# Kernel optimization log

Measured on AMD Instinct MI355X. Metric: run time of the kernel, lower is better.

The kernel has to match this reference:

```python
import jax, jax.numpy as jnp
import numpy as np

E = 7       # number of experts (len(expert_details))
K = 2       # top-k routing
CAP = 3072  # per-expert capacity ~ ceil(T*K/E * 1.25)
D = 1024    # d_model
H = 4096    # d_ff = 4*d_model
T = 8192    # tokens (B=2, S=4096)


def setup_inputs() -> dict:
    key = jax.random.key(0)
    k1, k2, k3, k4 = jax.random.split(key, 4)
    x = jax.random.normal(k1, (T, D), jnp.float32)
    Wg = jax.random.normal(k2, (D, E), jnp.float32) * 0.02
    W1 = jax.random.normal(k3, (E, D, H), jnp.float32) * 0.02
    W2 = jax.random.normal(k4, (E, H, D), jnp.float32) * 0.02
    return {"x": x, "Wg": Wg, "W1": W1, "W2": W2}


def reference(x, Wg, W1, W2):
    Tn, Dn = x.shape
    # --- router ---
    gates = jax.nn.softmax(x @ Wg, axis=-1)          # [T, E]
    topw, topi = jax.lax.top_k(gates, K)             # [T, K]
    topw = topw / jnp.sum(topw, axis=-1, keepdims=True)
    flat_e = topi.reshape(-1)                        # [T*K] expert ids (int)
    flat_w = topw.reshape(-1)                        # [T*K] combine weights
    # --- position within each expert (priority = token order) ---
    onehot = jax.nn.one_hot(flat_e, E, dtype=jnp.int32)           # [T*K, E]
    pos = jnp.sum(jnp.cumsum(onehot, axis=0) * onehot, axis=-1) - 1  # [T*K]
    keep = pos < CAP
    slot = jnp.where(keep, pos, CAP)  # overflow tokens go to pad slot CAP
    # --- dispatch: scatter tokens into [E, CAP, D] buffer ---
    x_rep = jnp.repeat(x, K, axis=0)                               # [T*K, D]
    buf = jnp.zeros((E, CAP + 1, Dn), x.dtype).at[flat_e, slot].set(x_rep)[:, :CAP]
    # --- grouped expert FFN (grouped GEMMs) ---
    h = jax.nn.gelu(jnp.einsum('ecd,edh->ech', buf, W1))
    y = jnp.einsum('ech,ehd->ecd', h, W2)                          # [E, CAP, D]
    # --- combine: gather back and weight ---
    y_pad = jnp.concatenate([y, jnp.zeros((E, 1, Dn), y.dtype)], axis=1)
    out_slots = y_pad[flat_e, slot] * (flat_w * keep.astype(flat_w.dtype))[:, None]
    return out_slots.reshape(Tn, K, Dn).sum(axis=1)                # [T, D]
```

## Files before the change

kernel.cpp:

```cpp
#include <hip/hip_runtime.h>
#include <stdint.h>


#define NEXP 7
#define KTOP 2
#define CAP 3072
#define DM 1024
#define HF 4096
#define TT 8192

typedef __bf16 bf16x8 __attribute__((ext_vector_type(8)));
typedef float f32x4 __attribute__((ext_vector_type(4)));

__device__ __forceinline__ unsigned short f2bf(float v) {
  union { float f; unsigned u; } a; a.f = v;
  unsigned r = a.u + 0x7FFFu + ((a.u >> 16) & 1u);
  return (unsigned short)(r >> 16);
}
__device__ __forceinline__ float bf2f(unsigned short h) {
  union { unsigned u; float f; } a; a.u = ((unsigned)h) << 16; return a.f;
}
__device__ __forceinline__ float gelu_t(float v) {
  float u = 0.7978845608028654f * (v + 0.044715f * v * v * v);
  float ex = __expf(2.0f * u);
  float th = 1.0f - 2.0f / (ex + 1.0f);
  return 0.5f * v * (1.0f + th);
}
__device__ __forceinline__ void gl2lds16(const void* g, void* l) {
  __builtin_amdgcn_global_load_lds(
      (const __attribute__((address_space(1))) unsigned int*)g,
      (__attribute__((address_space(3))) unsigned int*)l, 16, 0, 0);
}

__global__ void init_counts(int* counts) {
  if (threadIdx.x < NEXP) counts[threadIdx.x] = 0;
}

__global__ void router_kernel(const float* __restrict__ x, const float* __restrict__ Wg,
                              int* __restrict__ counts, int* __restrict__ flatE,
                              int* __restrict__ flatSlot, int* __restrict__ tokOfSlot,
                              float* __restrict__ wOfSlot) {
  int wave = threadIdx.x >> 6, lane = threadIdx.x & 63;
  int t = blockIdx.x * 4 + wave;
  double acc[NEXP];
#pragma unroll
  for (int e = 0; e < NEXP; ++e) acc[e] = 0.0;
  const float* xr = x + (long)t * DM;
  for (int j = 0; j < DM / 64; ++j) {
    int d = j * 64 + lane;
    double xv = (double)xr[d];
#pragma unroll
    for (int e = 0; e < NEXP; ++e) acc[e] += xv * (double)Wg[d * NEXP + e];
  }
#pragma unroll
  for (int e = 0; e < NEXP; ++e) {
#pragma unroll
    for (int off = 32; off > 0; off >>= 1) acc[e] += __shfl_down(acc[e], off);
  }
  if (lane == 0) {
    int i1 = 0; double l1 = acc[0];
    for (int e2 = 1; e2 < NEXP; ++e2) if (acc[e2] > l1) { l1 = acc[e2]; i1 = e2; }
    int i2 = -1; double l2 = -1e300;
    for (int e2 = 0; e2 < NEXP; ++e2) if (e2 != i1 && acc[e2] > l2) { l2 = acc[e2]; i2 = e2; }
    float w1 = (float)(1.0 / (1.0 + exp(l2 - l1)));
    float w2 = 1.0f - w1;
    int fi0 = t * 2, fi1 = t * 2 + 1;
    int p0 = atomicAdd(&counts[i1], 1);
    flatE[fi0] = i1; flatSlot[fi0] = (p0 < CAP) ? p0 : CAP;
    if (p0 < CAP) { tokOfSlot[i1 * CAP + p0] = fi0; wOfSlot[i1 * CAP + p0] = w1; }
    int p1 = atomicAdd(&counts[i2], 1);
    flatE[fi1] = i2; flatSlot[fi1] = (p1 < CAP) ? p1 : CAP;
    if (p1 < CAP) { tokOfSlot[i2 * CAP + p1] = fi1; wOfSlot[i2 * CAP + p1] = w2; }
  }
}

__global__ void transcvt(const float* __restrict__ in, unsigned short* __restrict__ out,
                         int R, int C) {
  __shared__ float tile[64][65];
  long base = (long)blockIdx.z * (long)R * (long)C;
  const float* inp = in + base;
  unsigned short* outp = out + base;
  int c0 = blockIdx.x * 64, r0 = blockIdx.y * 64;
  int lx = threadIdx.x & 63, ly = threadIdx.x >> 6;
#pragma unroll
  for (int i = 0; i < 16; ++i) {
    int r = ly + i * 4;
    tile[r][lx] = inp[(long)(r0 + r) * C + c0 + lx];
  }
  __syncthreads();
#pragma unroll
  for (int i = 0; i < 16; ++i) {
    int c = ly + i * 4;
    outp[(long)(c0 + c) * R + r0 + lx] = f2bf(tile[lx][c]);
  }
}

__global__ void scatter_x(const float* __restrict__ x, const int* __restrict__ flatE,
                          const int* __restrict__ flatSlot, unsigned short* __restrict__ xb) {
  int fi = blockIdx.x;
  int s = flatSlot[fi];
  if (s >= CAP) return;
  int e = flatE[fi];
  const float4* xr = (const float4*)(x + (long)(fi >> 1) * DM);
  float4 v = xr[threadIdx.x];
  ushort4 o; o.x = f2bf(v.x); o.y = f2bf(v.y); o.z = f2bf(v.z); o.w = f2bf(v.w);
  ((ushort4*)(xb + ((long)e * CAP + s) * DM))[threadIdx.x] = o;
}

template <int EPI>
__global__ __launch_bounds__(256, 2) void gemm_bt(
    const unsigned short* __restrict__ A, const unsigned short* __restrict__ Bt,
    void* __restrict__ Cout, const int* __restrict__ counts,
    const int* __restrict__ tokOfSlot, const float* __restrict__ wOfSlot,
    int K, int N, int eoff, long aexps, long cexps) {
  __shared__ unsigned short sA[128 * 32];
  __shared__ unsigned short sB[128 * 32];
  int e = eoff + blockIdx.z;
  int mcnt = counts[e]; mcnt = mcnt < CAP ? mcnt : CAP;
  int m0 = blockIdx.y * 128;
  if (m0 >= mcnt) return;
  int n0 = blockIdx.x * 128;
  const unsigned short* Ae = A + (long)blockIdx.z * aexps;
  const unsigned short* Be = Bt + (long)e * (long)N * (long)K;

  int tid = threadIdx.x;
  int lane = tid & 63, wave = tid >> 6;
  int lm = lane & 15, quad = lane >> 4;
  int wm = (wave & 1) * 64, wn = (wave >> 1) * 64;

  int ra = tid >> 2;
  int ca = (tid & 3) * 8;
  const unsigned short* Ab0 = Ae + (long)(m0 + ra) * K + ca;
  const unsigned short* Ab1 = Ae + (long)(m0 + 64 + ra) * K + ca;
  const unsigned short* Bb0 = Be + (long)(n0 + ra) * K + ca;
  const unsigned short* Bb1 = Be + (long)(n0 + 64 + ra) * K + ca;
  unsigned short* sAp0 = &sA[tid * 8];
  unsigned short* sAp1 = &sA[(tid + 256) * 8];
  unsigned short* sBp0 = &sB[tid * 8];
  unsigned short* sBp1 = &sB[(tid + 256) * 8];

  f32x4 acc[4][4];
#pragma unroll
  for (int i = 0; i < 4; ++i)
#pragma unroll
    for (int j = 0; j < 4; ++j) acc[i][j] = f32x4{0.f, 0.f, 0.f, 0.f};

  for (int k0 = 0; k0 < K; k0 += 32) {
    gl2lds16(Ab0 + k0, sAp0);
    gl2lds16(Ab1 + k0, sAp1);
    gl2lds16(Bb0 + k0, sBp0);
    gl2lds16(Bb1 + k0, sBp1);
    __syncthreads();
    bf16x8 aF[4], bF[4];
#pragma unroll
    for (int mi = 0; mi < 4; ++mi)
      aF[mi] = *(const bf16x8*)&sA[(wm + mi * 16 + lm) * 32 + quad * 8];
#pragma unroll
    for (int ni = 0; ni < 4; ++ni)
      bF[ni] = *(const bf16x8*)&sB[(wn + ni * 16 + lm) * 32 + quad * 8];
#pragma unroll
    for (int mi = 0; mi < 4; ++mi)
#pragma unroll
      for (int ni = 0; ni < 4; ++ni)
        acc[mi][ni] = __builtin_amdgcn_mfma_f32_16x16x32_bf16(aF[mi], bF[ni], acc[mi][ni], 0, 0, 0);
    __syncthreads();
  }

  if (EPI == 0) {
    unsigned short* Ce = (unsigned short*)Cout + (long)blockIdx.z * cexps;
#pragma unroll
    for (int mi = 0; mi < 4; ++mi) {
      int mb = m0 + wm + mi * 16 + quad * 4;
#pragma unroll
      for (int r = 0; r < 4; ++r) {
        int m = mb + r;
        if (m < mcnt) {
#pragma unroll
          for (int ni = 0; ni < 4; ++ni) {
            int n = n0 + wn + ni * 16 + lm;
            Ce[(long)m * N + n] = f2bf(gelu_t(acc[mi][ni][r]));
          }
        }
      }
    }
  } else {
    unsigned short* Y = (unsigned short*)Cout;
#pragma unroll
    for (int mi = 0; mi < 4; ++mi) {
      int mb = m0 + wm + mi * 16 + quad * 4;
#pragma unroll
      for (int r = 0; r < 4; ++r) {
        int m = mb + r;
        if (m < mcnt) {
          int fi = tokOfSlot[e * CAP + m];
          float w = wOfSlot[e * CAP + m];
#pragma unroll
          for (int ni = 0; ni < 4; ++ni) {
            int n = n0 + wn + ni * 16 + lm;
            Y[(long)fi * N + n] = f2bf(w * acc[mi][ni][r]);
          }
        }
      }
    }
  }
}

__global__ void combine_k(const unsigned short* __restrict__ yflat,
                          const int* __restrict__ flatSlot, float* __restrict__ out) {
  int t = blockIdx.x;
  bool k0 = flatSlot[2 * t] < CAP, k1 = flatSlot[2 * t + 1] < CAP;
  const ushort4* y0 = (const ushort4*)(yflat + (long)(2 * t) * DM);
  const ushort4* y1 = (const ushort4*)(yflat + (long)(2 * t + 1) * DM);
  ushort4 a = y0[threadIdx.x], b = y1[threadIdx.x];
  float4 r;
  r.x = (k0 ? bf2f(a.x) : 0.f) + (k1 ? bf2f(b.x) : 0.f);
  r.y = (k0 ? bf2f(a.y) : 0.f) + (k1 ? bf2f(b.y) : 0.f);
  r.z = (k0 ? bf2f(a.z) : 0.f) + (k1 ? bf2f(b.z) : 0.f);
  r.w = (k0 ? bf2f(a.w) : 0.f) + (k1 ? bf2f(b.w) : 0.f);
  ((float4*)(out + (long)t * DM))[threadIdx.x] = r;
}

extern "C" void kernel_launch(void* const* d_in, const int* in_sizes, int n_in,
                              void* d_out, int out_size, void* d_ws, size_t ws_size,
                              hipStream_t stream) {
  const float* x  = (const float*)d_in[0];
  const float* Wg = (const float*)d_in[1];
  const float* W1 = (const float*)d_in[2];
  const float* W2 = (const float*)d_in[3];
  float* out = (float*)d_out;

  char* ws = (char*)d_ws;
  size_t off = 0;
  auto alloc = [&](size_t b) { void* p = ws + off; off = (off + b + 255) & ~(size_t)255; return p; };
  int* counts            = (int*)alloc(NEXP * 4);
  int* flatE             = (int*)alloc((size_t)TT * KTOP * 4);
  int* flatSlot          = (int*)alloc((size_t)TT * KTOP * 4);
  int* tokOfSlot         = (int*)alloc((size_t)NEXP * CAP * 4);
  float* wOfSlot         = (float*)alloc((size_t)NEXP * CAP * 4);
  unsigned short* Wb1    = (unsigned short*)alloc((size_t)NEXP * DM * HF * 2);
  unsigned short* Wb2    = (unsigned short*)alloc((size_t)NEXP * DM * HF * 2);
  unsigned short* xb     = (unsigned short*)alloc((size_t)NEXP * CAP * DM * 2);
  unsigned short* yflat  = (unsigned short*)alloc((size_t)TT * KTOP * DM * 2);
  size_t hbA = (size_t)NEXP * CAP * HF * 2;
  size_t hbB = (size_t)CAP * HF * 2;
  int planA = (off + hbA) <= ws_size;
  unsigned short* hb = (unsigned short*)alloc(planA ? hbA : hbB);

  init_counts<<<1, 64, 0, stream>>>(counts);
  router_kernel<<<TT / 4, 256, 0, stream>>>(x, Wg, counts, flatE, flatSlot, tokOfSlot, wOfSlot);
  transcvt<<<dim3(HF / 64, DM / 64, NEXP), 256, 0, stream>>>(W1, Wb1, DM, HF);
  transcvt<<<dim3(DM / 64, HF / 64, NEXP), 256, 0, stream>>>(W2, Wb2, HF, DM);
  scatter_x<<<TT * KTOP, 256, 0, stream>>>(x, flatE, flatSlot, xb);

  if (planA) {
    gemm_bt<0><<<dim3(HF / 128, CAP / 128, NEXP), 256, 0, stream>>>(
        xb, Wb1, hb, counts, tokOfSlot, wOfSlot, DM, HF, 0, (long)CAP * DM, (long)CAP * HF);
    gemm_bt<1><<<dim3(DM / 128, CAP / 128, NEXP), 256, 0, stream>>>(
        hb, Wb2, yflat, counts, tokOfSlot, wOfSlot, HF, DM, 0, (long)CAP * HF, 0);
  } else {
    for (int e = 0; e < NEXP; ++e) {
      gemm_bt<0><<<dim3(HF / 128, CAP / 128, 1), 256, 0, stream>>>(
          xb + (size_t)e * CAP * DM, Wb1, hb, counts, tokOfSlot, wOfSlot, DM, HF, e, 0, 0);
      gemm_bt<1><<<dim3(DM / 128, CAP / 128, 1), 256, 0, stream>>>(
          hb, Wb2, yflat, counts, tokOfSlot, wOfSlot, HF, DM, e, 0, 0);
    }
  }
  combine_k<<<TT, 256, 0, stream>>>(yflat, flatSlot, out);
}
```

Before: 947.8 us.

## Remap GEMM tile order for XCD-aware locality and vectorize transpose stores

The GEMM grid is flattened into one dimension and tiles are remapped so that blocks with the same index modulo 8 (one per XCD under round-robin dispatch) walk along N for a fixed group of M rows. The goal is to improve L2 reuse of the A rows within each XCD. The weight transpose-convert kernel now writes 8 bf16 values per 16-byte vector store instead of scalar 2-byte stores. The init kernel is replaced by hipMemsetAsync. N becomes a compile-time template parameter.

```diff
diff --git a/kernel.cpp b/kernel.cpp
--- a/kernel.cpp
+++ b/kernel.cpp
@@ -11,6 +11,7 @@
 
 typedef __bf16 bf16x8 __attribute__((ext_vector_type(8)));
 typedef float f32x4 __attribute__((ext_vector_type(4)));
+typedef unsigned short ushort8_t __attribute__((ext_vector_type(8)));
 
 __device__ __forceinline__ unsigned short f2bf(float v) {
   union { float f; unsigned u; } a; a.f = v;
@@ -30,10 +31,6 @@
   __builtin_amdgcn_global_load_lds(
       (const __attribute__((address_space(1))) unsigned int*)g,
       (__attribute__((address_space(3))) unsigned int*)l, 16, 0, 0);
-}
-
-__global__ void init_counts(int* counts) {
-  if (threadIdx.x < NEXP) counts[threadIdx.x] = 0;
 }
 
 __global__ void router_kernel(const float* __restrict__ x, const float* __restrict__ Wg,
@@ -88,10 +85,15 @@
     tile[r][lx] = inp[(long)(r0 + r) * C + c0 + lx];
   }
   __syncthreads();
-#pragma unroll
-  for (int i = 0; i < 16; ++i) {
-    int c = ly + i * 4;
-    outp[(long)(c0 + c) * R + r0 + lx] = f2bf(tile[lx][c]);
+  int cl = threadIdx.x >> 3;
+  int rb = (threadIdx.x & 7) * 8;
+#pragma unroll
+  for (int h = 0; h < 2; ++h) {
+    int c = cl + 32 * h;
+    ushort8_t v;
+#pragma unroll
+    for (int j = 0; j < 8; ++j) v[j] = f2bf(tile[rb + j][c]);
+    *(ushort8_t*)&outp[(long)(c0 + c) * R + r0 + rb] = v;
   }
 }
 
@@ -107,19 +109,25 @@
   ((ushort4*)(xb + ((long)e * CAP + s) * DM))[threadIdx.x] = o;
 }
 
-template <int EPI>
+template <int EPI, int TN>
 __global__ __launch_bounds__(256, 2) void gemm_bt(
     const unsigned short* __restrict__ A, const unsigned short* __restrict__ Bt,
     void* __restrict__ Cout, const int* __restrict__ counts,
     const int* __restrict__ tokOfSlot, const float* __restrict__ wOfSlot,
-    int K, int N, int eoff, long aexps, long cexps) {
+    int K, int eoff, long aexps, long cexps) {
+  constexpr int N = TN * 128;
   __shared__ unsigned short sA[128 * 32];
   __shared__ unsigned short sB[128 * 32];
   int e = eoff + blockIdx.z;
   int mcnt = counts[e]; mcnt = mcnt < CAP ? mcnt : CAP;
-  int m0 = blockIdx.y * 128;
+  int bx = blockIdx.x;
+  int cls = bx & 7;
+  int step = bx >> 3;
+  int m_t = cls + 8 * (step / TN);
+  int n_t = step % TN;
+  int m0 = m_t * 128;
   if (m0 >= mcnt) return;
-  int n0 = blockIdx.x * 128;
+  int n0 = n_t * 128;
   const unsigned short* Ae = A + (long)blockIdx.z * aexps;
   const unsigned short* Be = Bt + (long)e * (long)N * (long)K;
 
@@ -246,23 +254,25 @@
   int planA = (off + hbA) <= ws_size;
   unsigned short* hb = (unsigned short*)alloc(planA ? hbA : hbB);
 
-  init_counts<<<1, 64, 0, stream>>>(counts);
+  constexpr int TM = CAP / 128;
+
+  hipMemsetAsync(counts, 0, NEXP * sizeof(int), stream);
   router_kernel<<<TT / 4, 256, 0, stream>>>(x, Wg, counts, flatE, flatSlot, tokOfSlot, wOfSlot);
   transcvt<<<dim3(HF / 64, DM / 64, NEXP), 256, 0, stream>>>(W1, Wb1, DM, HF);
   transcvt<<<dim3(DM / 64, HF / 64, NEXP), 256, 0, stream>>>(W2, Wb2, HF, DM);
   scatter_x<<<TT * KTOP, 256, 0, stream>>>(x, flatE, flatSlot, xb);
 
   if (planA) {
-    gemm_bt<0><<<dim3(HF / 128, CAP / 128, NEXP), 256, 0, stream>>>(
-        xb, Wb1, hb, counts, tokOfSlot, wOfSlot, DM, HF, 0, (long)CAP * DM, (long)CAP * HF);
-    gemm_bt<1><<<dim3(DM / 128, CAP / 128, NEXP), 256, 0, stream>>>(
-        hb, Wb2, yflat, counts, tokOfSlot, wOfSlot, HF, DM, 0, (long)CAP * HF, 0);
+    gemm_bt<0, HF / 128><<<dim3(TM * (HF / 128), 1, NEXP), 256, 0, stream>>>(
+        xb, Wb1, hb, counts, tokOfSlot, wOfSlot, DM, 0, (long)CAP * DM, (long)CAP * HF);
+    gemm_bt<1, DM / 128><<<dim3(TM * (DM / 128), 1, NEXP), 256, 0, stream>>>(
+        hb, Wb2, yflat, counts, tokOfSlot, wOfSlot, HF, 0, (long)CAP * HF, 0);
   } else {
     for (int e = 0; e < NEXP; ++e) {
-      gemm_bt<0><<<dim3(HF / 128, CAP / 128, 1), 256, 0, stream>>>(
-          xb + (size_t)e * CAP * DM, Wb1, hb, counts, tokOfSlot, wOfSlot, DM, HF, e, 0, 0);
-      gemm_bt<1><<<dim3(DM / 128, CAP / 128, 1), 256, 0, stream>>>(
-          hb, Wb2, yflat, counts, tokOfSlot, wOfSlot, HF, DM, e, 0, 0);
+      gemm_bt<0, HF / 128><<<dim3(TM * (HF / 128), 1, 1), 256, 0, stream>>>(
+          xb + (size_t)e * CAP * DM, Wb1, hb, counts, tokOfSlot, wOfSlot, DM, e, 0, 0);
+      gemm_bt<1, DM / 128><<<dim3(TM * (DM / 128), 1, 1), 256, 0, stream>>>(
+          hb, Wb2, yflat, counts, tokOfSlot, wOfSlot, HF, e, 0, 0);
     }
   }
   combine_k<<<TT, 256, 0, stream>>>(yflat, flatSlot, out);
```

After: 975.8 us. 1.03x slower.
